# Kernel optimization log

Hardware: AMD Instinct MI355X
Metric: run time of the kernel (lower is better)

## Reference

```python
import jax, jax.numpy as jnp
import numpy as np

FORGET_BIAS = 1.0

def _lstm_scan(x_seq, W, b, c0, h0):
    """x_seq: [T, B, D]; W: [D+H, 4H] (gate order i,j,f,o as in BasicLSTMCell)."""
    def step(carry, x_t):
        c, h = carry
        gates = jnp.dot(jnp.concatenate([x_t, h], axis=-1), W) + b  # [B, 4H]
        i, j, f, o = jnp.split(gates, 4, axis=-1)
        c_new = c * jax.nn.sigmoid(f + FORGET_BIAS) + jax.nn.sigmoid(i) * jnp.tanh(j)
        h_new = jnp.tanh(c_new) * jax.nn.sigmoid(o)
        return (c_new, h_new), h_new
    (c_T, h_T), hs = jax.lax.scan(step, (c0, h0), x_seq)
    return hs, (c_T, h_T)


def setup_inputs() -> dict:
    key = jax.random.key(0)
    ks = jax.random.split(key, 10)
    B, T_enc, D_in = 128, 64, 2048
    T_dec, D_w, H, V = 32, 300, 512, 32000
    s = lambda fan_in: 1.0 / np.sqrt(fan_in)
    return {
        "frames": jax.random.normal(ks[0], (B, T_enc, D_in), dtype=jnp.float32),
        "caption_ids": jax.random.randint(ks[1], (B, T_dec), 0, V, dtype=jnp.int32),
        "emb_table": jax.random.normal(ks[2], (V, D_w), dtype=jnp.float32) * 0.1,
        "W_enc": jax.random.normal(ks[3], (D_in + H, 4 * H), dtype=jnp.float32) * s(D_in + H),
        "b_enc": jnp.zeros((4 * H,), dtype=jnp.float32),
        "W_dec": jax.random.normal(ks[4], (D_w + H, 4 * H), dtype=jnp.float32) * s(D_w + H),
        "b_dec": jnp.zeros((4 * H,), dtype=jnp.float32),
        "W_out": jax.random.normal(ks[5], (H, D_w), dtype=jnp.float32) * s(H),
        "b_out": jnp.zeros((D_w,), dtype=jnp.float32),
    }


def reference(frames, caption_ids, emb_table, W_enc, b_enc, W_dec, b_dec, W_out, b_out):
    B, _, _ = frames.shape
    H = W_out.shape[0]
    c0 = jnp.zeros((B, H), dtype=frames.dtype)
    h0 = jnp.zeros((B, H), dtype=frames.dtype)

    # Encoder: dynamic_rnn over frames (dropout keep_prob=1 -> identity)
    _, enc_state = _lstm_scan(jnp.swapaxes(frames, 0, 1), W_enc, b_enc, c0, h0)

    # Decoder: teacher-forced over caption embeddings, starting from encoder state
    cap_emb = emb_table[caption_ids]                       # [B, T_dec, D_w]
    dec_hs, _ = _lstm_scan(jnp.swapaxes(cap_emb, 0, 1), W_dec, b_dec, *enc_state)  # [T_dec, B, H]

    # hidden_to_word dense per timestep
    word_vecs = jnp.einsum('tbh,hw->tbw', dec_hs, W_out) + b_out  # [T_dec, B, D_w]
    return jnp.swapaxes(word_vecs, 0, 1)                   # [B, T_dec, D_w]
```

## Files before the change

### kernel.cpp

```cpp
#include <hip/hip_runtime.h>
#include <stdint.h>

typedef unsigned short u16;
typedef __attribute__((ext_vector_type(4))) float f32x4;
typedef __attribute__((ext_vector_type(8))) short short8;
typedef __attribute__((ext_vector_type(4))) unsigned short u16x4;
typedef __attribute__((ext_vector_type(4))) int int4v;

__device__ __forceinline__ u16 f2b(float f) {
  uint32_t u = __float_as_uint(f);
  uint32_t r = (u + 0x7fffu + ((u >> 16) & 1u)) >> 16;
  return (u16)r;
}
__device__ __forceinline__ float b2f(u16 b) {
  return __uint_as_float(((uint32_t)b) << 16);
}
__device__ __forceinline__ float sigm(float x) { return 1.f / (1.f + __expf(-x)); }
__device__ __forceinline__ float tanh_fast(float x) {
  float e = __expf(2.f * x);
  return 1.f - 2.f / (e + 1.f);
}
__device__ __forceinline__ void gl2lds16(const void* g, void* l) {
  __builtin_amdgcn_global_load_lds((const __attribute__((address_space(1))) void*)g,
                                   (__attribute__((address_space(3))) void*)l, 16, 0, 0);
}

__global__ void cvt_bf16_kernel(const float* __restrict__ in, u16* __restrict__ out, int n4) {
  int i = blockIdx.x * 256 + threadIdx.x;
  if (i >= n4) return;
  float4 v = ((const float4*)in)[i];
  int e = i * 4;
  int b = e >> 17;
  int t = (e >> 11) & 63;
  int d = e & 2047;
  size_t row = (size_t)t * 128 + b;
  u16x4 o = { f2b(v.x), f2b(v.y), f2b(v.z), f2b(v.w) };
  *(u16x4*)(out + row * 2048 + d) = o;
}

__global__ void transpose_kernel(const float* __restrict__ W, u16* __restrict__ WT,
                                 int ldin, int ldout, int xreal, int xpad) {
  __shared__ float tile[64][65];
  const int kb = blockIdx.x * 64;
  const int pb = blockIdx.y * 64;
  const int t = threadIdx.x;
  const int pc = t & 63;
  const int kr4 = t >> 6;
#pragma unroll
  for (int it = 0; it < 16; ++it) {
    int kl = kr4 + it * 4;
    int kc = kb + kl;
    int ko = kc < xpad ? kc : kc - (xpad - xreal);
    bool valid = (kc < xreal) || (kc >= xpad);
    tile[kl][pc] = valid ? W[(size_t)ko * ldin + pb + pc] : 0.f;
  }
  __syncthreads();
  const int pl = t >> 2;
  const int kq = t & 3;
#pragma unroll
  for (int half = 0; half < 2; ++half) {
    union { short8 v; u16 a[8]; } pk;
#pragma unroll
    for (int i = 0; i < 8; ++i) pk.a[i] = f2b(tile[kq * 16 + half * 8 + i][pl]);
    *(short8*)&WT[(size_t)(pb + pl) * ldout + kb + kq * 16 + half * 8] = pk.v;
  }
}

__global__ void woutT_kernel(const float* __restrict__ Wout, u16* __restrict__ WT) {
  int idx = blockIdx.x * 256 + threadIdx.x;
  if (idx >= 384 * 512) return;
  int n = idx >> 9, k = idx & 511;
  float v = (n < 300) ? Wout[(size_t)k * 300 + n] : 0.f;
  WT[idx] = f2b(v);
}

__global__ void embed_kernel(const int* __restrict__ ids, const float* __restrict__ emb,
                             u16* __restrict__ Adec) {
  int r = blockIdx.x;
  int t = r >> 7, b = r & 127;
  int id = ids[b * 32 + t];
  const float* src = emb + (size_t)id * 300;
  u16* dst = Adec + (size_t)r * 320;
  for (int d = threadIdx.x; d < 320; d += 64)
    dst[d] = f2b(d < 300 ? src[d] : 0.f);
}

struct SmemLstm { u16 wlds[128][520]; u16 stage[2][16][32]; };
struct SmemGemm { u16 at[2][128 * 32]; u16 bt[2][128 * 32]; };
union SmemU { SmemLstm l; SmemGemm g; };

__global__ __launch_bounds__(256)
void mega_kernel(const u16* __restrict__ A_enc, const u16* __restrict__ WencT,
                 u16* __restrict__ pre_enc, const float* __restrict__ b_enc,
                 const u16* __restrict__ A_dec, const u16* __restrict__ WdecT,
                 u16* __restrict__ pre_dec, const float* __restrict__ b_dec,
                 int* __restrict__ hbuf, u16* __restrict__ dec_hs,
                 int* __restrict__ flags, int* __restrict__ pf_enc,
                 int* __restrict__ pf_dec) {
  __shared__ SmemU sm;
  const int bid = blockIdx.x;
  const int tid = threadIdx.x;
  const int lane = tid & 63;

  if (bid < 128) {
    const int hb = tid >> 6;
    const int bg = bid & 7;
    const int hg = bid >> 3;
    const int colq = lane & 15;
    const int rquad = lane >> 4;

    for (int i = tid; i < 128 * 64; i += 256) {
      int lr = i >> 6, cc = i & 63;
      const u16* src = WencT + (size_t)((lr >> 5) * 512 + hg * 32 + (lr & 31)) * 2560 + 2048;
      *(short8*)&sm.l.wlds[lr][cc * 8] = *(const short8*)(src + cc * 8);
    }
    __syncthreads();

    float cst[4] = {0.f, 0.f, 0.f, 0.f};
    const int brow = bg * 16 + rquad * 4;
    const int pbase = hg * 32 + (hb & 1) * 16 + colq;
    union HV { int4v i; short8 s; };

    for (int s = 0; s < 96; ++s) {
      const bool dec = (s >= 64);
      const int sb = s & 1;
      if (hb < 2) {
        const u16* pre_t = dec ? (pre_dec + (size_t)(s - 64) * 262144)
                               : (pre_enc + (size_t)s * 262144);
        int* pf = dec ? (pf_dec + (s - 64)) : (pf_enc + s);
        while (__hip_atomic_load(pf, __ATOMIC_RELAXED, __HIP_MEMORY_SCOPE_AGENT) != 16) {}
        asm volatile("" ::: "memory");
        int praw[4][4];
        const u16* p0 = pre_t + (size_t)brow * 2048 + pbase;
#pragma unroll
        for (int l = 0; l < 4; ++l)
#pragma unroll
          for (int r = 0; r < 4; ++r)
            asm volatile("global_load_ushort %0, %1, off sc0 sc1"
                         : "=v"(praw[l][r]) : "v"(p0 + (size_t)r * 2048 + l * 512) : "memory");
        if (s > 0) {
          const int* fp = flags + ((size_t)s * 8 + bg) * 16 + (lane & 15);
          while (__hip_atomic_load(fp, __ATOMIC_RELAXED, __HIP_MEMORY_SCOPE_AGENT) == 0) {}
          asm volatile("" ::: "memory");
        }
        HV hv[16];
        const int* hread = hbuf + (size_t)s * 32768 + bg * 4096 + colq * 16 + rquad * 4;
#pragma unroll
        for (int g = 0; g < 4; ++g) {
          const int* hp = hread + g * 1024;
#pragma unroll
          for (int q = 0; q < 4; ++q)
            asm volatile("global_load_dwordx4 %0, %1, off offset:%2 sc0 sc1"
                         : "=v"(hv[g * 4 + q].i) : "v"(hp), "i"(q * 1024) : "memory");
        }
        asm volatile("s_waitcnt vmcnt(0)" ::: "memory");
        __builtin_amdgcn_sched_barrier(0);
#pragma unroll
        for (int kt = 0; kt < 16; ++kt) asm volatile("" : "+v"(hv[kt].i));
#pragma unroll
        for (int l = 0; l < 4; ++l)
#pragma unroll
          for (int r = 0; r < 4; ++r) asm volatile("" : "+v"(praw[l][r]));
        f32x4 acc[4];
#pragma unroll
        for (int l = 0; l < 4; ++l)
#pragma unroll
          for (int r = 0; r < 4; ++r) acc[l][r] = b2f((u16)praw[l][r]);
#pragma unroll
        for (int kt = 0; kt < 16; ++kt) {
#pragma unroll
          for (int l = 0; l < 4; ++l) {
            short8 bf = *(const short8*)&sm.l.wlds[l * 32 + hb * 16 + colq][kt * 32 + rquad * 8];
            acc[l] = __builtin_amdgcn_mfma_f32_16x16x32_bf16(hv[kt].s, bf, acc[l], 0, 0, 0);
          }
        }
#pragma unroll
        for (int r = 0; r < 4; ++r) {
          float iv = acc[0][r], jv = acc[1][r], fv = acc[2][r], ov = acc[3][r];
          float cn = cst[r] * sigm(fv + 1.f) + sigm(iv) * tanh_fast(jv);
          cst[r] = cn;
          float hvv = tanh_fast(cn) * sigm(ov);
          sm.l.stage[sb][rquad * 4 + r][hb * 16 + colq] = f2b(hvv);
        }
      }
      __syncthreads();
      if (hb == 2) {
        const int t2 = tid - 128;
        const int row = t2 >> 2, q = t2 & 3;
        union { short8 v; int4v i; } vv;
        vv.v = *(const short8*)&sm.l.stage[sb][row][q * 8];
        int* dst = hbuf + (size_t)(s + 1) * 32768 + bg * 4096 + hg * 256 + row * 16 + q * 4;
        asm volatile("global_store_dwordx4 %0, %1, off sc0 sc1"
                     :: "v"(dst), "v"(vv.i) : "memory");
        if (dec)
          *(short8*)&dec_hs[(size_t)(s - 64) * 65536 + (size_t)(bg * 16 + row) * 512 +
                            hg * 32 + q * 8] = vv.v;
        asm volatile("s_waitcnt vmcnt(0)" ::: "memory");
        if (t2 == 0) {
          int* fp = flags + ((size_t)(s + 1) * 8 + bg) * 16 + hg;
          int one = 1;
          asm volatile("global_store_dword %0, %1, off sc0 sc1"
                       :: "v"(fp), "v"(one) : "memory");
        }
      }
      if (s == 63) {
        for (int i = tid; i < 128 * 64; i += 256) {
          int lr = i >> 6, cc = i & 63;
          const u16* src = WdecT + (size_t)((lr >> 5) * 512 + hg * 32 + (lr & 31)) * 832 + 320;
          *(short8*)&sm.l.wlds[lr][cc * 8] = *(const short8*)(src + cc * 8);
        }
        __syncthreads();
      }
    }
    asm volatile("s_waitcnt vmcnt(0)" ::: "memory");
    return;
  }

  int idx = bid - 128;
  const u16* A; const u16* BT; u16* C; const float* bias; int* flag;
  int lda, ldb, K, m0, n0;
  if (idx < 1024) {
    int t = idx >> 4, nt = idx & 15;
    A = A_enc; lda = 2048; BT = WencT; ldb = 2560; K = 2048;
    C = pre_enc; bias = b_enc; flag = pf_enc + t;
    m0 = t * 128; n0 = nt * 128;
  } else {
    idx -= 1024;
    int t = idx >> 4, nt = idx & 15;
    A = A_dec; lda = 320; BT = WdecT; ldb = 832; K = 320;
    C = pre_dec; bias = b_dec; flag = pf_dec + t;
    m0 = t * 128; n0 = nt * 128;
  }
  const int wave = tid >> 6;
  const int wm = wave & 1, wn = wave >> 1;
  const int colq = lane & 15, rquad = lane >> 4;

  f32x4 acc[4][4];
#pragma unroll
  for (int i = 0; i < 4; ++i)
#pragma unroll
    for (int j = 0; j < 4; ++j) { f32x4 z = {0.f, 0.f, 0.f, 0.f}; acc[i][j] = z; }

  auto stage_tile = [&](int buf, int k0) {
#pragma unroll
    for (int c = 0; c < 2; ++c) {
      const int ch = wave + c * 4;
      const int slot = ch * 64 + lane;
      const int m = slot >> 2;
      const int koff = (slot & 3) * 8;
      gl2lds16(A + (size_t)(m0 + m) * lda + k0 + koff, sm.g.at[buf] + ch * 512);
      gl2lds16(BT + (size_t)(n0 + m) * ldb + k0 + koff, sm.g.bt[buf] + ch * 512);
    }
  };

  stage_tile(0, 0);
  __builtin_amdgcn_s_waitcnt(0);
  __syncthreads();
  const int niter = K >> 5;
  for (int it = 0; it < niter; ++it) {
    const int cur = it & 1;
    if (it + 1 < niter) stage_tile(cur ^ 1, (it + 1) << 5);
    short8 af[4], bf[4];
#pragma unroll
    for (int i = 0; i < 4; ++i)
      af[i] = *(const short8*)(sm.g.at[cur] + (wm * 64 + i * 16 + colq) * 32 + rquad * 8);
#pragma unroll
    for (int j = 0; j < 4; ++j)
      bf[j] = *(const short8*)(sm.g.bt[cur] + (wn * 64 + j * 16 + colq) * 32 + rquad * 8);
#pragma unroll
    for (int i = 0; i < 4; ++i)
#pragma unroll
      for (int j = 0; j < 4; ++j)
        acc[i][j] = __builtin_amdgcn_mfma_f32_16x16x32_bf16(af[i], bf[j], acc[i][j], 0, 0, 0);
    __builtin_amdgcn_s_waitcnt(0);
    __syncthreads();
  }

  const int gm_base = m0 + wm * 64;
  const int gn_base = n0 + wn * 64;
#pragma unroll
  for (int i = 0; i < 4; ++i) {
#pragma unroll
    for (int j = 0; j < 4; ++j) {
      const int gn = gn_base + j * 16 + colq;
      const float bv = bias[gn];
      const int rbase = gm_base + i * 16 + rquad * 4;
#pragma unroll
      for (int r = 0; r < 4; ++r) {
        int hv16 = (int)f2b(acc[i][j][r] + bv);
        const u16* addr = C + (size_t)(rbase + r) * 2048 + gn;
        asm volatile("global_store_short %0, %1, off sc0 sc1"
                     :: "v"(addr), "v"(hv16) : "memory");
      }
    }
  }
  asm volatile("s_waitcnt vmcnt(0)" ::: "memory");
  __syncthreads();
  if (tid == 0)
    __hip_atomic_fetch_add(flag, 1, __ATOMIC_RELAXED, __HIP_MEMORY_SCOPE_AGENT);
}

__global__ __launch_bounds__(256)
void out_gemm_kernel(const u16* __restrict__ A, const u16* __restrict__ BT,
                     float* __restrict__ Cv, const float* __restrict__ bias) {
  const int lda = 512, ldb = 512, K = 512;
  __shared__ u16 atile[128 * 32];
  __shared__ u16 btile[128 * 32];
  const int tid = threadIdx.x;
  const int wave = tid >> 6;
  const int lane = tid & 63;
  const int m0 = blockIdx.x * 128;
  const int n0 = blockIdx.y * 128;
  const int wm = wave & 1;
  const int wn = wave >> 1;
  const int colq = lane & 15;
  const int rquad = lane >> 4;

  f32x4 acc[4][4];
#pragma unroll
  for (int i = 0; i < 4; ++i)
#pragma unroll
    for (int j = 0; j < 4; ++j) { f32x4 z = {0.f, 0.f, 0.f, 0.f}; acc[i][j] = z; }

  for (int k0 = 0; k0 < K; k0 += 32) {
#pragma unroll
    for (int c = 0; c < 2; ++c) {
      const int ch = wave + c * 4;
      const int slot = ch * 64 + lane;
      const int m = slot >> 2;
      const int koff = (slot & 3) * 8;
      gl2lds16(A + (size_t)(m0 + m) * lda + k0 + koff, atile + ch * 512);
      gl2lds16(BT + (size_t)(n0 + m) * ldb + k0 + koff, btile + ch * 512);
    }
    __builtin_amdgcn_s_waitcnt(0);
    __syncthreads();
    short8 af[4], bf[4];
#pragma unroll
    for (int i = 0; i < 4; ++i)
      af[i] = *(const short8*)(atile + (wm * 64 + i * 16 + colq) * 32 + rquad * 8);
#pragma unroll
    for (int j = 0; j < 4; ++j)
      bf[j] = *(const short8*)(btile + (wn * 64 + j * 16 + colq) * 32 + rquad * 8);
#pragma unroll
    for (int i = 0; i < 4; ++i)
#pragma unroll
      for (int j = 0; j < 4; ++j)
        acc[i][j] = __builtin_amdgcn_mfma_f32_16x16x32_bf16(af[i], bf[j], acc[i][j], 0, 0, 0);
    __syncthreads();
  }

  const int gm_base = m0 + wm * 64;
  const int gn_base = n0 + wn * 64;
#pragma unroll
  for (int i = 0; i < 4; ++i) {
#pragma unroll
    for (int j = 0; j < 4; ++j) {
      const int gn = gn_base + j * 16 + colq;
      const float bv = (gn < 300) ? bias[gn] : 0.f;
      const int rbase = gm_base + i * 16 + rquad * 4;
#pragma unroll
      for (int r = 0; r < 4; ++r) {
        const float v = acc[i][j][r] + bv;
        const int row = rbase + r;
        if (gn < 300)
          Cv[(size_t)((row & 127) * 32 + (row >> 7)) * 300 + gn] = v;
      }
    }
  }
}

extern "C" void kernel_launch(void* const* d_in, const int* in_sizes, int n_in,
                              void* d_out, int out_size, void* d_ws, size_t ws_size,
                              hipStream_t stream) {
  const float* frames = (const float*)d_in[0];
  const int* cap_ids  = (const int*)d_in[1];
  const float* emb    = (const float*)d_in[2];
  const float* W_enc  = (const float*)d_in[3];
  const float* b_enc  = (const float*)d_in[4];
  const float* W_dec  = (const float*)d_in[5];
  const float* b_dec  = (const float*)d_in[6];
  const float* W_out  = (const float*)d_in[7];
  const float* b_out  = (const float*)d_in[8];
  float* out = (float*)d_out;

  char* ws = (char*)d_ws;
  size_t off = 0;
  auto alloc = [&](size_t bytes) {
    void* p = ws + off;
    off += (bytes + 255) & ~(size_t)255;
    return p;
  };
  u16* A_enc   = (u16*)alloc(8192ull * 2048 * 2);
  u16* WencT   = (u16*)alloc(2048ull * 2560 * 2);
  u16* pre_enc = (u16*)alloc(64ull * 128 * 2048 * 2);
  u16* A_dec   = (u16*)alloc(4096ull * 320 * 2);
  u16* WdecT   = (u16*)alloc(2048ull * 832 * 2);
  u16* pre_dec = (u16*)alloc(32ull * 128 * 2048 * 2);
  u16* WoutT   = (u16*)alloc(384ull * 512 * 2);
  u16* dec_hs  = (u16*)alloc(32ull * 128 * 512 * 2);
  int* hbuf    = (int*)alloc(97ull * 32768 * 4);
  int* flags   = (int*)alloc(97ull * 8 * 16 * 4);
  int* pf      = (int*)alloc(96ull * 4);
  int* pf_enc  = pf;
  int* pf_dec  = pf + 64;

  hipMemsetAsync(hbuf, 0, 32768ull * 4, stream);
  hipMemsetAsync(flags, 0, 97ull * 8 * 16 * 4, stream);
  hipMemsetAsync(pf, 0, 96ull * 4, stream);

  cvt_bf16_kernel<<<16384, 256, 0, stream>>>(frames, A_enc, 4194304);
  transpose_kernel<<<dim3(40, 32), 256, 0, stream>>>(W_enc, WencT, 2048, 2560, 2048, 2048);
  transpose_kernel<<<dim3(13, 32), 256, 0, stream>>>(W_dec, WdecT, 2048, 832, 300, 320);
  woutT_kernel<<<768, 256, 0, stream>>>(W_out, WoutT);
  embed_kernel<<<4096, 64, 0, stream>>>(cap_ids, emb, A_dec);

  mega_kernel<<<1664, 256, 0, stream>>>(A_enc, WencT, pre_enc, b_enc,
                                        A_dec, WdecT, pre_dec, b_dec,
                                        hbuf, dec_hs, flags, pf_enc, pf_dec);

  out_gemm_kernel<<<dim3(32, 3), 256, 0, stream>>>(dec_hs, WoutT, out, b_out);
}
```

Before: 727.2 us.

## Fuse prep kernels, fold output GEMM into mega kernel, deepen GEMM pipeline

Merges the five preprocessing kernels into a single prep_kernel launch. The output projection GEMM moves into the persistent mega_kernel as extra blocks that wait on per-timestep decoder flags, so it overlaps with the recurrence. The tiled GEMM changes from double to quad buffering, waiting on partial vmcnt counts. The LSTM loop also prefetches the next step's readiness flag to skip spinning. The trade-offs are more shared memory, added flag polling from the output blocks, and a risk of deadlock if those blocks get scheduled ahead of the producer blocks.

```diff
diff --git a/kernel.cpp b/kernel.cpp
--- a/kernel.cpp
+++ b/kernel.cpp
@@ -25,68 +25,85 @@
                                    (__attribute__((address_space(3))) void*)l, 16, 0, 0);
 }
 
-__global__ void cvt_bf16_kernel(const float* __restrict__ in, u16* __restrict__ out, int n4) {
-  int i = blockIdx.x * 256 + threadIdx.x;
-  if (i >= n4) return;
-  float4 v = ((const float4*)in)[i];
-  int e = i * 4;
-  int b = e >> 17;
-  int t = (e >> 11) & 63;
-  int d = e & 2047;
-  size_t row = (size_t)t * 128 + b;
-  u16x4 o = { f2b(v.x), f2b(v.y), f2b(v.z), f2b(v.w) };
-  *(u16x4*)(out + row * 2048 + d) = o;
-}
-
-__global__ void transpose_kernel(const float* __restrict__ W, u16* __restrict__ WT,
-                                 int ldin, int ldout, int xreal, int xpad) {
+__global__ __launch_bounds__(256)
+void prep_kernel(const float* __restrict__ frames, u16* __restrict__ A_enc,
+                 const float* __restrict__ W_enc, u16* __restrict__ WencT,
+                 const float* __restrict__ W_dec, u16* __restrict__ WdecT,
+                 const float* __restrict__ W_out, u16* __restrict__ WoutT,
+                 const int* __restrict__ ids, const float* __restrict__ emb,
+                 u16* __restrict__ Adec) {
   __shared__ float tile[64][65];
-  const int kb = blockIdx.x * 64;
-  const int pb = blockIdx.y * 64;
-  const int t = threadIdx.x;
-  const int pc = t & 63;
-  const int kr4 = t >> 6;
-#pragma unroll
-  for (int it = 0; it < 16; ++it) {
-    int kl = kr4 + it * 4;
-    int kc = kb + kl;
-    int ko = kc < xpad ? kc : kc - (xpad - xreal);
-    bool valid = (kc < xreal) || (kc >= xpad);
-    tile[kl][pc] = valid ? W[(size_t)ko * ldin + pb + pc] : 0.f;
-  }
-  __syncthreads();
-  const int pl = t >> 2;
-  const int kq = t & 3;
-#pragma unroll
-  for (int half = 0; half < 2; ++half) {
-    union { short8 v; u16 a[8]; } pk;
-#pragma unroll
-    for (int i = 0; i < 8; ++i) pk.a[i] = f2b(tile[kq * 16 + half * 8 + i][pl]);
-    *(short8*)&WT[(size_t)(pb + pl) * ldout + kb + kq * 16 + half * 8] = pk.v;
-  }
-}
-
-__global__ void woutT_kernel(const float* __restrict__ Wout, u16* __restrict__ WT) {
-  int idx = blockIdx.x * 256 + threadIdx.x;
-  if (idx >= 384 * 512) return;
-  int n = idx >> 9, k = idx & 511;
-  float v = (n < 300) ? Wout[(size_t)k * 300 + n] : 0.f;
-  WT[idx] = f2b(v);
-}
-
-__global__ void embed_kernel(const int* __restrict__ ids, const float* __restrict__ emb,
-                             u16* __restrict__ Adec) {
-  int r = blockIdx.x;
+  const int bid = blockIdx.x;
+  const int tid = threadIdx.x;
+
+  if (bid < 16384) {
+    int i = bid * 256 + tid;
+    float4 v = ((const float4*)frames)[i];
+    int e = i * 4;
+    int b = e >> 17;
+    int t = (e >> 11) & 63;
+    int d = e & 2047;
+    size_t row = (size_t)t * 128 + b;
+    u16x4 o = { f2b(v.x), f2b(v.y), f2b(v.z), f2b(v.w) };
+    *(u16x4*)(A_enc + row * 2048 + d) = o;
+    return;
+  }
+
+  const float* W; u16* WT; int ldin, ldout, xreal, xpad, bx, by;
+  if (bid < 18080) {
+    if (bid < 17664) {
+      int idx = bid - 16384;
+      W = W_enc; WT = WencT; ldin = 2048; ldout = 2560; xreal = 2048; xpad = 2048;
+      bx = idx % 40; by = idx / 40;
+    } else {
+      int idx = bid - 17664;
+      W = W_dec; WT = WdecT; ldin = 2048; ldout = 832; xreal = 300; xpad = 320;
+      bx = idx % 13; by = idx / 13;
+    }
+    const int kb = bx * 64;
+    const int pb = by * 64;
+    const int pc = tid & 63;
+    const int kr4 = tid >> 6;
+#pragma unroll
+    for (int it = 0; it < 16; ++it) {
+      int kl = kr4 + it * 4;
+      int kc = kb + kl;
+      int ko = kc < xpad ? kc : kc - (xpad - xreal);
+      bool valid = (kc < xreal) || (kc >= xpad);
+      tile[kl][pc] = valid ? W[(size_t)ko * ldin + pb + pc] : 0.f;
+    }
+    __syncthreads();
+    const int pl = tid >> 2;
+    const int kq = tid & 3;
+#pragma unroll
+    for (int half = 0; half < 2; ++half) {
+      union { short8 v; u16 a[8]; } pk;
+#pragma unroll
+      for (int i = 0; i < 8; ++i) pk.a[i] = f2b(tile[kq * 16 + half * 8 + i][pl]);
+      *(short8*)&WT[(size_t)(pb + pl) * ldout + kb + kq * 16 + half * 8] = pk.v;
+    }
+    return;
+  }
+
+  if (bid < 18848) {
+    int idx = (bid - 18080) * 256 + tid;
+    int n = idx >> 9, k = idx & 511;
+    float v = (n < 300) ? W_out[(size_t)k * 300 + n] : 0.f;
+    WoutT[idx] = f2b(v);
+    return;
+  }
+
+  int r = (bid - 18848) * 4 + (tid >> 6);
   int t = r >> 7, b = r & 127;
   int id = ids[b * 32 + t];
   const float* src = emb + (size_t)id * 300;
   u16* dst = Adec + (size_t)r * 320;
-  for (int d = threadIdx.x; d < 320; d += 64)
+  for (int d = tid & 63; d < 320; d += 64)
     dst[d] = f2b(d < 300 ? src[d] : 0.f);
 }
 
 struct SmemLstm { u16 wlds[128][520]; u16 stage[2][16][32]; };
-struct SmemGemm { u16 at[2][128 * 32]; u16 bt[2][128 * 32]; };
+struct SmemGemm { u16 at[4][128 * 32]; u16 bt[4][128 * 32]; };
 union SmemU { SmemLstm l; SmemGemm g; };
 
 __global__ __launch_bounds__(256)
@@ -94,6 +111,8 @@
                  u16* __restrict__ pre_enc, const float* __restrict__ b_enc,
                  const u16* __restrict__ A_dec, const u16* __restrict__ WdecT,
                  u16* __restrict__ pre_dec, const float* __restrict__ b_dec,
+                 const u16* __restrict__ WoutT, const float* __restrict__ b_out,
+                 float* __restrict__ outp,
                  int* __restrict__ hbuf, u16* __restrict__ dec_hs,
                  int* __restrict__ flags, int* __restrict__ pf_enc,
                  int* __restrict__ pf_dec) {
@@ -120,6 +139,7 @@
     const int brow = bg * 16 + rquad * 4;
     const int pbase = hg * 32 + (hb & 1) * 16 + colq;
     union HV { int4v i; short8 s; };
+    int pf_next = 0;
 
     for (int s = 0; s < 96; ++s) {
       const bool dec = (s >= 64);
@@ -127,8 +147,10 @@
       if (hb < 2) {
         const u16* pre_t = dec ? (pre_dec + (size_t)(s - 64) * 262144)
                                : (pre_enc + (size_t)s * 262144);
-        int* pf = dec ? (pf_dec + (s - 64)) : (pf_enc + s);
-        while (__hip_atomic_load(pf, __ATOMIC_RELAXED, __HIP_MEMORY_SCOPE_AGENT) != 16) {}
+        if (pf_next != 16) {
+          int* pf = dec ? (pf_dec + (s - 64)) : (pf_enc + s);
+          while (__hip_atomic_load(pf, __ATOMIC_RELAXED, __HIP_MEMORY_SCOPE_AGENT) != 16) {}
+        }
         asm volatile("" ::: "memory");
         int praw[4][4];
         const u16* p0 = pre_t + (size_t)brow * 2048 + pbase;
@@ -152,6 +174,10 @@
           for (int q = 0; q < 4; ++q)
             asm volatile("global_load_dwordx4 %0, %1, off offset:%2 sc0 sc1"
                          : "=v"(hv[g * 4 + q].i) : "v"(hp), "i"(q * 1024) : "memory");
+        }
+        if (s + 1 < 96) {
+          const int* pfn = (s + 1 >= 64) ? (pf_dec + (s + 1 - 64)) : (pf_enc + (s + 1));
+          pf_next = __hip_atomic_load(pfn, __ATOMIC_RELAXED, __HIP_MEMORY_SCOPE_AGENT);
         }
         asm volatile("s_waitcnt vmcnt(0)" ::: "memory");
         __builtin_amdgcn_sched_barrier(0);
@@ -192,9 +218,12 @@
         int* dst = hbuf + (size_t)(s + 1) * 32768 + bg * 4096 + hg * 256 + row * 16 + q * 4;
         asm volatile("global_store_dwordx4 %0, %1, off sc0 sc1"
                      :: "v"(dst), "v"(vv.i) : "memory");
-        if (dec)
-          *(short8*)&dec_hs[(size_t)(s - 64) * 65536 + (size_t)(bg * 16 + row) * 512 +
-                            hg * 32 + q * 8] = vv.v;
+        if (dec) {
+          const u16* da = dec_hs + (size_t)(s - 64) * 65536 +
+                          (size_t)(bg * 16 + row) * 512 + hg * 32 + q * 8;
+          asm volatile("global_store_dwordx4 %0, %1, off sc0 sc1"
+                       :: "v"(da), "v"(vv.i) : "memory");
+        }
         asm volatile("s_waitcnt vmcnt(0)" ::: "memory");
         if (t2 == 0) {
           int* fp = flags + ((size_t)(s + 1) * 8 + bg) * 16 + hg;
@@ -217,19 +246,28 @@
   }
 
   int idx = bid - 128;
-  const u16* A; const u16* BT; u16* C; const float* bias; int* flag;
-  int lda, ldb, K, m0, n0;
+  const u16* A; const u16* BT; u16* Cb = nullptr; const float* bias; int* flag = nullptr;
+  int lda, ldb, K, m0, n0, mode, tcap = 0;
   if (idx < 1024) {
     int t = idx >> 4, nt = idx & 15;
     A = A_enc; lda = 2048; BT = WencT; ldb = 2560; K = 2048;
-    C = pre_enc; bias = b_enc; flag = pf_enc + t;
-    m0 = t * 128; n0 = nt * 128;
-  } else {
+    Cb = pre_enc; bias = b_enc; flag = pf_enc + t;
+    m0 = t * 128; n0 = nt * 128; mode = 0;
+  } else if (idx < 1536) {
     idx -= 1024;
     int t = idx >> 4, nt = idx & 15;
     A = A_dec; lda = 320; BT = WdecT; ldb = 832; K = 320;
-    C = pre_dec; bias = b_dec; flag = pf_dec + t;
-    m0 = t * 128; n0 = nt * 128;
+    Cb = pre_dec; bias = b_dec; flag = pf_dec + t;
+    m0 = t * 128; n0 = nt * 128; mode = 0;
+  } else {
+    idx -= 1536;
+    int t = idx / 3, nt = idx % 3;
+    A = dec_hs; lda = 512; BT = WoutT; ldb = 512; K = 512;
+    bias = b_out; m0 = t * 128; n0 = nt * 128; mode = 1; tcap = t;
+    const int* wf = flags + (size_t)(tcap + 65) * 128 + (tid & 127);
+    while (__hip_atomic_load(wf, __ATOMIC_RELAXED, __HIP_MEMORY_SCOPE_AGENT) == 0) {}
+    asm volatile("" ::: "memory");
+    __syncthreads();
   }
   const int wave = tid >> 6;
   const int wm = wave & 1, wn = wave >> 1;
@@ -253,13 +291,20 @@
     }
   };
 
+  const int niter = K >> 5;
   stage_tile(0, 0);
-  __builtin_amdgcn_s_waitcnt(0);
-  __syncthreads();
-  const int niter = K >> 5;
+  stage_tile(1, 32);
+  stage_tile(2, 64);
   for (int it = 0; it < niter; ++it) {
-    const int cur = it & 1;
-    if (it + 1 < niter) stage_tile(cur ^ 1, (it + 1) << 5);
+    if (it + 3 < niter) stage_tile((it + 3) & 3, (it + 3) << 5);
+    const int excess = (niter - 1 - it) < 3 ? (niter - 1 - it) : 3;
+    if (excess == 3)      asm volatile("s_waitcnt vmcnt(12)" ::: "memory");
+    else if (excess == 2) asm volatile("s_waitcnt vmcnt(8)" ::: "memory");
+    else if (excess == 1) asm volatile("s_waitcnt vmcnt(4)" ::: "memory");
+    else                  asm volatile("s_waitcnt vmcnt(0)" ::: "memory");
+    __builtin_amdgcn_s_barrier();
+    __builtin_amdgcn_sched_barrier(0);
+    const int cur = it & 3;
     short8 af[4], bf[4];
 #pragma unroll
     for (int i = 0; i < 4; ++i)
@@ -272,98 +317,49 @@
 #pragma unroll
       for (int j = 0; j < 4; ++j)
         acc[i][j] = __builtin_amdgcn_mfma_f32_16x16x32_bf16(af[i], bf[j], acc[i][j], 0, 0, 0);
-    __builtin_amdgcn_s_waitcnt(0);
-    __syncthreads();
+    __builtin_amdgcn_sched_barrier(0);
+    asm volatile("s_waitcnt lgkmcnt(0)" ::: "memory");
+    __builtin_amdgcn_s_barrier();
   }
 
   const int gm_base = m0 + wm * 64;
   const int gn_base = n0 + wn * 64;
-#pragma unroll
-  for (int i = 0; i < 4; ++i) {
-#pragma unroll
-    for (int j = 0; j < 4; ++j) {
-      const int gn = gn_base + j * 16 + colq;
-      const float bv = bias[gn];
-      const int rbase = gm_base + i * 16 + rquad * 4;
-#pragma unroll
-      for (int r = 0; r < 4; ++r) {
-        int hv16 = (int)f2b(acc[i][j][r] + bv);
-        const u16* addr = C + (size_t)(rbase + r) * 2048 + gn;
-        asm volatile("global_store_short %0, %1, off sc0 sc1"
-                     :: "v"(addr), "v"(hv16) : "memory");
+  if (mode == 0) {
+#pragma unroll
+    for (int i = 0; i < 4; ++i) {
+#pragma unroll
+      for (int j = 0; j < 4; ++j) {
+        const int gn = gn_base + j * 16 + colq;
+        const float bv = bias[gn];
+        const int rbase = gm_base + i * 16 + rquad * 4;
+#pragma unroll
+        for (int r = 0; r < 4; ++r) {
+          int hv16 = (int)f2b(acc[i][j][r] + bv);
+          const u16* addr = Cb + (size_t)(rbase + r) * 2048 + gn;
+          asm volatile("global_store_short %0, %1, off sc0 sc1"
+                       :: "v"(addr), "v"(hv16) : "memory");
+        }
       }
     }
-  }
-  asm volatile("s_waitcnt vmcnt(0)" ::: "memory");
-  __syncthreads();
-  if (tid == 0)
-    __hip_atomic_fetch_add(flag, 1, __ATOMIC_RELAXED, __HIP_MEMORY_SCOPE_AGENT);
-}
-
-__global__ __launch_bounds__(256)
-void out_gemm_kernel(const u16* __restrict__ A, const u16* __restrict__ BT,
-                     float* __restrict__ Cv, const float* __restrict__ bias) {
-  const int lda = 512, ldb = 512, K = 512;
-  __shared__ u16 atile[128 * 32];
-  __shared__ u16 btile[128 * 32];
-  const int tid = threadIdx.x;
-  const int wave = tid >> 6;
-  const int lane = tid & 63;
-  const int m0 = blockIdx.x * 128;
-  const int n0 = blockIdx.y * 128;
-  const int wm = wave & 1;
-  const int wn = wave >> 1;
-  const int colq = lane & 15;
-  const int rquad = lane >> 4;
-
-  f32x4 acc[4][4];
-#pragma unroll
-  for (int i = 0; i < 4; ++i)
-#pragma unroll
-    for (int j = 0; j < 4; ++j) { f32x4 z = {0.f, 0.f, 0.f, 0.f}; acc[i][j] = z; }
-
-  for (int k0 = 0; k0 < K; k0 += 32) {
-#pragma unroll
-    for (int c = 0; c < 2; ++c) {
-      const int ch = wave + c * 4;
-      const int slot = ch * 64 + lane;
-      const int m = slot >> 2;
-      const int koff = (slot & 3) * 8;
-      gl2lds16(A + (size_t)(m0 + m) * lda + k0 + koff, atile + ch * 512);
-      gl2lds16(BT + (size_t)(n0 + m) * ldb + k0 + koff, btile + ch * 512);
-    }
-    __builtin_amdgcn_s_waitcnt(0);
+    asm volatile("s_waitcnt vmcnt(0)" ::: "memory");
     __syncthreads();
-    short8 af[4], bf[4];
-#pragma unroll
-    for (int i = 0; i < 4; ++i)
-      af[i] = *(const short8*)(atile + (wm * 64 + i * 16 + colq) * 32 + rquad * 8);
-#pragma unroll
-    for (int j = 0; j < 4; ++j)
-      bf[j] = *(const short8*)(btile + (wn * 64 + j * 16 + colq) * 32 + rquad * 8);
-#pragma unroll
-    for (int i = 0; i < 4; ++i)
-#pragma unroll
-      for (int j = 0; j < 4; ++j)
-        acc[i][j] = __builtin_amdgcn_mfma_f32_16x16x32_bf16(af[i], bf[j], acc[i][j], 0, 0, 0);
-    __syncthreads();
-  }
-
-  const int gm_base = m0 + wm * 64;
-  const int gn_base = n0 + wn * 64;
-#pragma unroll
-  for (int i = 0; i < 4; ++i) {
-#pragma unroll
-    for (int j = 0; j < 4; ++j) {
-      const int gn = gn_base + j * 16 + colq;
-      const float bv = (gn < 300) ? bias[gn] : 0.f;
-      const int rbase = gm_base + i * 16 + rquad * 4;
-#pragma unroll
-      for (int r = 0; r < 4; ++r) {
-        const float v = acc[i][j][r] + bv;
-        const int row = rbase + r;
-        if (gn < 300)
-          Cv[(size_t)((row & 127) * 32 + (row >> 7)) * 300 + gn] = v;
+    if (tid == 0)
+      __hip_atomic_fetch_add(flag, 1, __ATOMIC_RELAXED, __HIP_MEMORY_SCOPE_AGENT);
+  } else {
+#pragma unroll
+    for (int i = 0; i < 4; ++i) {
+#pragma unroll
+      for (int j = 0; j < 4; ++j) {
+        const int gn = gn_base + j * 16 + colq;
+        const float bv = (gn < 300) ? bias[gn] : 0.f;
+        const int rbase = gm_base + i * 16 + rquad * 4;
+#pragma unroll
+        for (int r = 0; r < 4; ++r) {
+          const float v = acc[i][j][r] + bv;
+          const int row = rbase + r;
+          if (gn < 300)
+            outp[(size_t)((row & 127) * 32 + (row >> 7)) * 300 + gn] = v;
+        }
       }
     }
   }
@@ -408,15 +404,11 @@
   hipMemsetAsync(flags, 0, 97ull * 8 * 16 * 4, stream);
   hipMemsetAsync(pf, 0, 96ull * 4, stream);
 
-  cvt_bf16_kernel<<<16384, 256, 0, stream>>>(frames, A_enc, 4194304);
-  transpose_kernel<<<dim3(40, 32), 256, 0, stream>>>(W_enc, WencT, 2048, 2560, 2048, 2048);
-  transpose_kernel<<<dim3(13, 32), 256, 0, stream>>>(W_dec, WdecT, 2048, 832, 300, 320);
-  woutT_kernel<<<768, 256, 0, stream>>>(W_out, WoutT);
-  embed_kernel<<<4096, 64, 0, stream>>>(cap_ids, emb, A_dec);
-
-  mega_kernel<<<1664, 256, 0, stream>>>(A_enc, WencT, pre_enc, b_enc,
+  prep_kernel<<<19872, 256, 0, stream>>>(frames, A_enc, W_enc, WencT, W_dec, WdecT,
+                                         W_out, WoutT, cap_ids, emb, A_dec);
+
+  mega_kernel<<<1760, 256, 0, stream>>>(A_enc, WencT, pre_enc, b_enc,
                                         A_dec, WdecT, pre_dec, b_dec,
+                                        WoutT, b_out, out,
                                         hbuf, dec_hs, flags, pf_enc, pf_dec);
-
-  out_gemm_kernel<<<dim3(32, 3), 256, 0, stream>>>(dec_hs, WoutT, out, b_out);
-}
+}
```

After: 667.3 us. 1.09x faster.
